# Kernel tuning notes

Measured on AMD Instinct MI355X. Metric: run time of the kernel, lower is better.

## Reference

```python
import jax, jax.numpy as jnp
import numpy as np

K = 16          # top-k per pooled row
EPS = 1e-12     # tf.nn.l2_normalize epsilon


def setup_inputs() -> dict:
    key = jax.random.key(0)
    x = jax.random.normal(key, (16, 256, 128, 128), dtype=jnp.float32)
    return {"x": x}


def reference(x) -> tuple:
    # x: [B, C, H, W]; last_n_dims = 2 -> pool the trailing H*W axis.
    B, C, H, W = x.shape
    flat = x.reshape(B, C, H * W)                       # [B, C, HW]
    # tf.nn.l2_normalize(axis=-1): x / sqrt(max(sum(x^2), eps))
    sq = jnp.sum(flat * flat, axis=-1, keepdims=True)
    normed = flat * jax.lax.rsqrt(jnp.maximum(sq, EPS))  # [B, C, HW]
    top_k_value, top_k_idx = jax.lax.top_k(normed, K)    # [B, C, K]
    # decode flat indices into (h, w) coordinates (div/mod loop in original)
    h = top_k_idx // W
    w = top_k_idx % W
    coors = jnp.stack([h, w], axis=-1).astype(jnp.int32)  # [B, C, K, 2]
    return top_k_value, coors
```

## Files before the change

kernel.cpp:

```cpp
#include <hip/hip_runtime.h>


#define KSEL 16
#define HW   16384
#define WDIM 128
#define CAP  1024
#define T0   2.5f
#define NROWS 4096
#define VALS_TOTAL (NROWS * KSEL)

__device__ __forceinline__ void push_cand(unsigned long long* cand,
                                          unsigned* cnt, float v, int idx) {
    unsigned u = __float_as_uint(v);
    unsigned m = u ^ (((unsigned)((int)u >> 31)) | 0x80000000u);
    unsigned long long p =
        ((unsigned long long)m << 32) | (unsigned)(16383 - idx);
    unsigned slot = atomicAdd(cnt, 1u);
    if (slot < CAP) cand[slot] = p;
}

__global__ __launch_bounds__(256) void topk_rows(const float* __restrict__ x,
                                                 float* __restrict__ out) {
    const int row = blockIdx.x;
    const int t   = threadIdx.x;

    __shared__ unsigned long long s_cand[CAP];
    __shared__ unsigned s_cnt;
    __shared__ float s_part[4];
    __shared__ float s_scale;

    if (t == 0) s_cnt = 0;
    __syncthreads();

    const float4* rowp = (const float4*)(x + (size_t)row * HW);

    float T = T0;
    float sumsq = 0.0f;
    #pragma unroll
    for (int k = 0; k < 16; ++k) {
        float4 f = rowp[k * 256 + t];
        int base = k * 1024 + t * 4;
        sumsq = fmaf(f.x, f.x, sumsq);
        sumsq = fmaf(f.y, f.y, sumsq);
        sumsq = fmaf(f.z, f.z, sumsq);
        sumsq = fmaf(f.w, f.w, sumsq);
        if (f.x > T) push_cand(s_cand, &s_cnt, f.x, base + 0);
        if (f.y > T) push_cand(s_cand, &s_cnt, f.y, base + 1);
        if (f.z > T) push_cand(s_cand, &s_cnt, f.z, base + 2);
        if (f.w > T) push_cand(s_cand, &s_cnt, f.w, base + 3);
    }

    #pragma unroll
    for (int off = 32; off > 0; off >>= 1)
        sumsq += __shfl_down(sumsq, off, 64);
    if ((t & 63) == 0) s_part[t >> 6] = sumsq;
    __syncthreads();
    if (t == 0) {
        float tot = s_part[0] + s_part[1] + s_part[2] + s_part[3];
        s_scale = 1.0f / sqrtf(fmaxf(tot, 1e-12f));
    }
    unsigned cnt = s_cnt;

    float lo = -3.0e38f, hi = 3.0e38f;
    for (int it = 0; it < 24 && (cnt < KSEL || cnt > CAP); ++it) {
        if (cnt < KSEL) { hi = T; T = (lo < -1.0e38f) ? T - 1.0f : 0.5f * (lo + T); }
        else            { lo = T; T = (hi >  1.0e38f) ? T + 1.0f : 0.5f * (T + hi); }
        __syncthreads();
        if (t == 0) s_cnt = 0;
        __syncthreads();
        for (int k = 0; k < 16; ++k) {
            float4 f = rowp[k * 256 + t];
            int base = k * 1024 + t * 4;
            if (f.x > T) push_cand(s_cand, &s_cnt, f.x, base + 0);
            if (f.y > T) push_cand(s_cand, &s_cnt, f.y, base + 1);
            if (f.z > T) push_cand(s_cand, &s_cnt, f.z, base + 2);
            if (f.w > T) push_cand(s_cand, &s_cnt, f.w, base + 3);
        }
        __syncthreads();
        cnt = s_cnt;
    }
    if (cnt > CAP) cnt = CAP;
    __syncthreads();
    const float scale = s_scale;

    for (unsigned i = t; i < cnt; i += 256) {
        unsigned long long p = s_cand[i];
        unsigned m = (unsigned)(p >> 32);
        unsigned u = (m & 0x80000000u) ? (m ^ 0x80000000u) : ~m;
        float vn = __uint_as_float(u) * scale;
        unsigned u2 = __float_as_uint(vn);
        unsigned m2 = u2 ^ (((unsigned)((int)u2 >> 31)) | 0x80000000u);
        s_cand[i] = ((unsigned long long)m2 << 32) | (p & 0xFFFFFFFFull);
    }
    __syncthreads();

    for (unsigned i = t; i < cnt; i += 256) {
        unsigned long long p = s_cand[i];
        int rank = 0;
        for (unsigned j = 0; j < cnt; ++j) rank += (s_cand[j] > p) ? 1 : 0;
        if (rank < KSEL) {
            unsigned m = (unsigned)(p >> 32);
            unsigned u = (m & 0x80000000u) ? (m ^ 0x80000000u) : ~m;
            float vn = __uint_as_float(u);
            int idx = 16383 - (int)(unsigned)(p & 0xFFFFFFFFull);
            out[row * KSEL + rank] = vn;
            float* coor = out + VALS_TOTAL + ((size_t)row * KSEL + rank) * 2;
            coor[0] = (float)(idx >> 7);
            coor[1] = (float)(idx & (WDIM - 1));
        }
    }
}

extern "C" void kernel_launch(void* const* d_in, const int* in_sizes, int n_in,
                              void* d_out, int out_size, void* d_ws, size_t ws_size,
                              hipStream_t stream) {
    const float* x = (const float*)d_in[0];
    float* out = (float*)d_out;
    topk_rows<<<NROWS, 256, 0, stream>>>(x, out);
}
```

Baseline: 394.5 us.

## Keep row in registers and aggregate candidate atomics per wavefront

Each thread now loads its 64 row values into a register buffer once, and threshold retries reuse that buffer instead of rereading global memory. Candidate pushes use a wavefront ballot with a single leader atomicAdd and a prefix popcount, replacing one shared-memory atomic per element. The cost is higher register pressure from the 16 float4 buffer, which may reduce occupancy. The first filtering pass now runs after the sum of squares instead of being fused with it.

```diff
diff --git a/kernel.cpp b/kernel.cpp
--- a/kernel.cpp
+++ b/kernel.cpp
@@ -9,78 +9,82 @@
 #define NROWS 4096
 #define VALS_TOTAL (NROWS * KSEL)
 
-__device__ __forceinline__ void push_cand(unsigned long long* cand,
-                                          unsigned* cnt, float v, int idx) {
-    unsigned u = __float_as_uint(v);
-    unsigned m = u ^ (((unsigned)((int)u >> 31)) | 0x80000000u);
-    unsigned long long p =
-        ((unsigned long long)m << 32) | (unsigned)(16383 - idx);
-    unsigned slot = atomicAdd(cnt, 1u);
-    if (slot < CAP) cand[slot] = p;
-}
-
 __global__ __launch_bounds__(256) void topk_rows(const float* __restrict__ x,
                                                  float* __restrict__ out) {
-    const int row = blockIdx.x;
-    const int t   = threadIdx.x;
+    const int row  = blockIdx.x;
+    const int t    = threadIdx.x;
+    const int lane = t & 63;
 
     __shared__ unsigned long long s_cand[CAP];
     __shared__ unsigned s_cnt;
     __shared__ float s_part[4];
     __shared__ float s_scale;
 
-    if (t == 0) s_cnt = 0;
-    __syncthreads();
-
     const float4* rowp = (const float4*)(x + (size_t)row * HW);
 
-    float T = T0;
+    float4 buf[16];
+    #pragma unroll
+    for (int k = 0; k < 16; ++k) buf[k] = rowp[k * 256 + t];
+
     float sumsq = 0.0f;
     #pragma unroll
     for (int k = 0; k < 16; ++k) {
-        float4 f = rowp[k * 256 + t];
-        int base = k * 1024 + t * 4;
-        sumsq = fmaf(f.x, f.x, sumsq);
-        sumsq = fmaf(f.y, f.y, sumsq);
-        sumsq = fmaf(f.z, f.z, sumsq);
-        sumsq = fmaf(f.w, f.w, sumsq);
-        if (f.x > T) push_cand(s_cand, &s_cnt, f.x, base + 0);
-        if (f.y > T) push_cand(s_cand, &s_cnt, f.y, base + 1);
-        if (f.z > T) push_cand(s_cand, &s_cnt, f.z, base + 2);
-        if (f.w > T) push_cand(s_cand, &s_cnt, f.w, base + 3);
+        sumsq = fmaf(buf[k].x, buf[k].x, sumsq);
+        sumsq = fmaf(buf[k].y, buf[k].y, sumsq);
+        sumsq = fmaf(buf[k].z, buf[k].z, sumsq);
+        sumsq = fmaf(buf[k].w, buf[k].w, sumsq);
     }
-
     #pragma unroll
     for (int off = 32; off > 0; off >>= 1)
         sumsq += __shfl_down(sumsq, off, 64);
-    if ((t & 63) == 0) s_part[t >> 6] = sumsq;
+    if (lane == 0) s_part[t >> 6] = sumsq;
     __syncthreads();
     if (t == 0) {
         float tot = s_part[0] + s_part[1] + s_part[2] + s_part[3];
         s_scale = 1.0f / sqrtf(fmaxf(tot, 1e-12f));
     }
-    unsigned cnt = s_cnt;
 
-    float lo = -3.0e38f, hi = 3.0e38f;
-    for (int it = 0; it < 24 && (cnt < KSEL || cnt > CAP); ++it) {
-        if (cnt < KSEL) { hi = T; T = (lo < -1.0e38f) ? T - 1.0f : 0.5f * (lo + T); }
-        else            { lo = T; T = (hi >  1.0e38f) ? T + 1.0f : 0.5f * (T + hi); }
+    float T = T0, lo = -3.0e38f, hi = 3.0e38f;
+    unsigned cnt = 0;
+    for (int attempt = 0; attempt < 25; ++attempt) {
         __syncthreads();
         if (t == 0) s_cnt = 0;
         __syncthreads();
+        #pragma unroll
         for (int k = 0; k < 16; ++k) {
-            float4 f = rowp[k * 256 + t];
-            int base = k * 1024 + t * 4;
-            if (f.x > T) push_cand(s_cand, &s_cnt, f.x, base + 0);
-            if (f.y > T) push_cand(s_cand, &s_cnt, f.y, base + 1);
-            if (f.z > T) push_cand(s_cand, &s_cnt, f.z, base + 2);
-            if (f.w > T) push_cand(s_cand, &s_cnt, f.w, base + 3);
+            #pragma unroll
+            for (int c = 0; c < 4; ++c) {
+                float v = (c == 0) ? buf[k].x : (c == 1) ? buf[k].y
+                        : (c == 2) ? buf[k].z : buf[k].w;
+                bool p = v > T;
+                unsigned long long m = __ballot(p);
+                if (m) {
+                    int nb  = __popcll(m);
+                    int ldr = (int)__builtin_ctzll(m);
+                    unsigned base = 0;
+                    if (lane == ldr) base = atomicAdd(&s_cnt, (unsigned)nb);
+                    base = (unsigned)__shfl((int)base, ldr, 64);
+                    if (p) {
+                        unsigned pos = base +
+                            (unsigned)__popcll(m & ((1ull << lane) - 1ull));
+                        if (pos < CAP) {
+                            unsigned u  = __float_as_uint(v);
+                            unsigned mm = u ^ (((unsigned)((int)u >> 31)) | 0x80000000u);
+                            int idx = k * 1024 + t * 4 + c;
+                            s_cand[pos] = ((unsigned long long)mm << 32) |
+                                          (unsigned)(16383 - idx);
+                        }
+                    }
+                }
+            }
         }
         __syncthreads();
         cnt = s_cnt;
+        if (cnt >= KSEL && cnt <= CAP) break;
+        if (cnt < KSEL) { hi = T; T = (lo < -1.0e38f) ? T - 1.0f : 0.5f * (lo + T); }
+        else            { lo = T; T = (hi >  1.0e38f) ? T + 1.0f : 0.5f * (T + hi); }
     }
     if (cnt > CAP) cnt = CAP;
-    __syncthreads();
     const float scale = s_scale;
 
     for (unsigned i = t; i < cnt; i += 256) {
```

After: 361.3 us. 8.4% less time.
